# Optimization experiments

Measured on AMD Instinct MI355X. Metric: run time of the kernel, lower is better.

The kernel has to match this reference:

```python
import jax, jax.numpy as jnp
import numpy as np

DIM = 1024
HEADS = 16
HEAD_DIM = DIM // HEADS
SCALE = HEAD_DIM ** -0.5


def setup_inputs() -> dict:
    key = jax.random.key(0)
    ks = jax.random.split(key, 7)
    B, N, M = 2, 2048, 2048
    x = jax.random.normal(ks[0], (B, N, DIM), dtype=jnp.float32)
    y = jax.random.normal(ks[1], (B, M, DIM), dtype=jnp.float32)
    s = DIM ** -0.5
    Wq = jax.random.normal(ks[2], (DIM, DIM), dtype=jnp.float32) * s
    Wk = jax.random.normal(ks[3], (DIM, DIM), dtype=jnp.float32) * s
    Wv = jax.random.normal(ks[4], (DIM, DIM), dtype=jnp.float32) * s
    Wp = jax.random.normal(ks[5], (DIM, DIM), dtype=jnp.float32) * s
    bp = jax.random.normal(ks[6], (DIM,), dtype=jnp.float32) * 0.01
    return {"x": x, "y": y, "Wq": Wq, "Wk": Wk, "Wv": Wv, "Wp": Wp, "bp": bp}


def _split_heads(t):
    b, n, _ = t.shape
    return t.reshape(b, n, HEADS, HEAD_DIM).transpose(0, 2, 1, 3)  # b h n d


def reference(x, y, Wq, Wk, Wv, Wp, bp):
    q = _split_heads(x @ Wq)  # [b,h,n,d]
    k = _split_heads(y @ Wk)  # [b,h,m,d]
    v = _split_heads(y @ Wv)  # [b,h,m,d]
    attn = jnp.einsum('bhid,bhjd->bhij', q, k) * SCALE  # [b,h,n,m]
    attn = jax.nn.softmax(attn, axis=-1)
    out = jnp.einsum('bhij,bhjd->bhid', attn, v)  # [b,h,n,d]
    b, h, n, d = out.shape
    out = out.transpose(0, 2, 1, 3).reshape(b, n, h * d)  # [b,n,dim]
    return out @ Wp + bp
```

## Files before the change

### kernel.cpp

```cpp
#include <hip/hip_runtime.h>
#include <hip/hip_bf16.h>
#include <cstdint>

#define DIM   1024
#define HEADS 16
#define HDIM  64
#define BATCH 2
#define SEQ   2048
#define ROWS  (BATCH*SEQ)
static constexpr float QSCALE = 0.18033688f;

typedef float  f32x4  __attribute__((ext_vector_type(4)));
typedef float  f32x16 __attribute__((ext_vector_type(16)));
typedef float  float4v __attribute__((ext_vector_type(4)));
typedef __bf16 bf16x8 __attribute__((ext_vector_type(8)));
typedef __bf16 bf16x4 __attribute__((ext_vector_type(4)));
typedef __bf16 bf16x2 __attribute__((ext_vector_type(2)));
typedef unsigned u32x4v __attribute__((ext_vector_type(4)));

__device__ __forceinline__ void glds16(const __bf16* g, __bf16* l) {
  __builtin_amdgcn_global_load_lds(
      (const __attribute__((address_space(1))) void*)g,
      (__attribute__((address_space(3))) void*)l, 16, 0, 0);
}

__device__ __forceinline__ void wait_dma0() {
  asm volatile("s_waitcnt vmcnt(0) lgkmcnt(0)" ::: "memory");
}

__global__ __launch_bounds__(256) void prep_kernel(
    const float* __restrict__ x, const float* __restrict__ y,
    const float* __restrict__ Wq, const float* __restrict__ Wk,
    const float* __restrict__ Wv, const float* __restrict__ Wp,
    __bf16* __restrict__ xb, __bf16* __restrict__ yb, __bf16* __restrict__ Wt) {
  const int z = blockIdx.z, t = threadIdx.x;
  const size_t NEL = (size_t)ROWS * DIM;
  if (z < 8) {
    size_t idx = (((size_t)z * 1024 + blockIdx.x) * 256 + t) * 4;
    const float* s; __bf16* d;
    if (idx < NEL) { s = x + idx; d = xb + idx; }
    else           { s = y + (idx - NEL); d = yb + (idx - NEL); }
    const float4v v = *(const float4v*)s;
    bf16x4 o;
    o[0] = (__bf16)v[0]; o[1] = (__bf16)v[1]; o[2] = (__bf16)v[2]; o[3] = (__bf16)v[3];
    *(bf16x4*)d = o;
    return;
  }
  const int w = blockIdx.x >> 8, rem = blockIdx.x & 255;
  const float* W = (w == 0) ? Wq : (w == 1) ? Wk : (w == 2) ? Wv : Wp;
  __bf16* dst = Wt + (size_t)w * DIM * DIM;
  const int n0 = (rem & 15) * 64, k0 = (rem >> 4) * 64;
  __shared__ float T[64][65];
  const int col = t & 63, rw = t >> 6;
  #pragma unroll
  for (int p = 0; p < 16; ++p) {
    const int row = p * 4 + rw;
    T[row][col] = W[(size_t)(k0 + row) * DIM + n0 + col];
  }
  __syncthreads();
  #pragma unroll
  for (int p = 0; p < 16; ++p) {
    const int row = p * 4 + rw;
    dst[(size_t)(n0 + row) * DIM + k0 + col] = (__bf16)T[col][row];
  }
}

__global__ __launch_bounds__(256) void proj_kernel(
    const __bf16* __restrict__ xb, const __bf16* __restrict__ yb,
    const __bf16* __restrict__ Wt,
    __bf16* __restrict__ Qb, __bf16* __restrict__ Kb, __bf16* __restrict__ VT) {
  const int z = blockIdx.z;
  const __bf16* A = (z == 0) ? xb : yb;
  const __bf16* Bt = Wt + (size_t)z * DIM * DIM;

  __shared__ __bf16 S[2][128 * 64];
  __bf16* As = S[0];
  __bf16* Bs = S[1];

  const int t = threadIdx.x, lane = t & 63, wave = t >> 6;
  const int l15 = lane & 15, quad = lane >> 4;
  const int wm = wave & 1, wn = wave >> 1;
  const int rowBase = blockIdx.y * 128, colBase = blockIdx.x * 128;
  const int srow = lane >> 3;
  const int scol = ((lane & 7) ^ srow) * 8;

  f32x4 acc[4][4] = {};

  for (int kb = 0; kb < DIM; kb += 64) {
    __syncthreads();
    #pragma unroll
    for (int i = 0; i < 4; ++i) {
      const int c = wave * 4 + i;
      const int row = c * 8 + srow;
      glds16(&A[(size_t)(rowBase + row) * DIM + kb + scol], &As[c * 512]);
      glds16(&Bt[(size_t)(colBase + row) * DIM + kb + scol], &Bs[c * 512]);
    }
    __syncthreads();
    #pragma unroll
    for (int ks = 0; ks < 2; ++ks) {
      bf16x8 a[4], b[4];
      #pragma unroll
      for (int mi = 0; mi < 4; ++mi) {
        const int row = wm * 64 + mi * 16 + l15;
        a[mi] = *(const bf16x8*)&As[row * 64 + (((ks << 2) | quad) ^ (row & 7)) * 8];
      }
      #pragma unroll
      for (int ni = 0; ni < 4; ++ni) {
        const int row = wn * 64 + ni * 16 + l15;
        b[ni] = *(const bf16x8*)&Bs[row * 64 + (((ks << 2) | quad) ^ (row & 7)) * 8];
      }
      #pragma unroll
      for (int mi = 0; mi < 4; ++mi)
        #pragma unroll
        for (int ni = 0; ni < 4; ++ni)
          acc[mi][ni] = __builtin_amdgcn_mfma_f32_16x16x32_bf16(a[mi], b[ni], acc[mi][ni], 0, 0, 0);
    }
  }

  if (z < 2) {
    __bf16* out = (z == 0) ? Qb : Kb;
    const float sc = (z == 0) ? QSCALE : 1.0f;
    #pragma unroll
    for (int mi = 0; mi < 4; ++mi) {
      const int row0 = rowBase + wm * 64 + mi * 16 + quad * 4;
      #pragma unroll
      for (int ni = 0; ni < 4; ++ni) {
        const int col = colBase + wn * 64 + ni * 16 + l15;
        #pragma unroll
        for (int r = 0; r < 4; ++r)
          out[(size_t)(row0 + r) * DIM + col] = (__bf16)(acc[mi][ni][r] * sc);
      }
    }
    return;
  }

  __syncthreads();
  __bf16* Ts = &S[0][0];
  #pragma unroll
  for (int mi = 0; mi < 4; ++mi) {
    const int bk3 = wm * 8 + mi * 2 + (quad >> 1);
    #pragma unroll
    for (int ni = 0; ni < 4; ++ni) {
      const int dl = wn * 64 + ni * 16 + l15;
      bf16x4 pk;
      #pragma unroll
      for (int r = 0; r < 4; ++r) pk[r] = (__bf16)acc[mi][ni][r];
      *(bf16x4*)&Ts[dl * 128 + (bk3 ^ (dl & 7)) * 8 + (quad & 1) * 4] = pk;
    }
  }
  __syncthreads();
  const int d = t >> 1, khh = t & 1;
  const size_t vrow = (size_t)((rowBase >> 11) * HEADS * HDIM) + colBase + d;
  const int key0g = rowBase & (SEQ - 1);
  #pragma unroll
  for (int j = 0; j < 8; ++j) {
    const int kc = khh * 8 + j;
    const int lc = (kc & 8) | ((kc ^ d) & 7);
    const bf16x8 v = *(const bf16x8*)&Ts[d * 128 + lc * 8];
    *(bf16x8*)&VT[vrow * SEQ + key0g + kc * 8] = v;
  }
}

__global__ __launch_bounds__(256, 2) void attn_kernel(
    const __bf16* __restrict__ Qb, const __bf16* __restrict__ Kb,
    const __bf16* __restrict__ VT, __bf16* __restrict__ Ob) {
  __shared__ __bf16 KV[2][2][64 * 64];

  const int t = threadIdx.x, lane = t & 63, wave = t >> 6;
  const int x = lane & 31, hi = lane >> 5;
  const int bh = blockIdx.y, b = bh >> 4, h = bh & 15;
  const int qbase = blockIdx.x * 128 + wave * 32;
  const int srow = lane >> 3;
  const int scol = ((lane & 7) ^ srow) * 8;

  const __bf16* Kbh = Kb + (size_t)b * SEQ * DIM + h * HDIM;
  const __bf16* Vbh = VT + (size_t)bh * HDIM * SEQ;

  bf16x8 qf[4];
  #pragma unroll
  for (int kd = 0; kd < 4; ++kd)
    qf[kd] = *(const bf16x8*)&Qb[(size_t)(b * SEQ + qbase + x) * DIM
                                 + h * HDIM + kd * 16 + hi * 8];

  f32x16 o0 = {}, o1 = {};
  float lsum = 0.f;

  const int he16 = (hi ^ (x & 7)) << 4;
  const int rowb = x * 128;

  auto stage = [&](int jb, int buf) {
    #pragma unroll
    for (int i = 0; i < 2; ++i) {
      const int c = wave * 2 + i;
      const int row = c * 8 + srow;
      glds16(&Kbh[(size_t)(jb + row) * DIM + scol], &KV[buf][0][c * 512]);
      glds16(&Vbh[(size_t)row * SEQ + jb + scol], &KV[buf][1][c * 512]);
    }
  };

  stage(0, 0);
  for (int j = 0; j < SEQ / 64; ++j) {
    const int buf = j & 1;
    wait_dma0();
    __syncthreads();
    if (j + 1 < SEQ / 64) stage((j + 1) * 64, buf ^ 1);
    const char* Ks = (const char*)KV[buf][0];
    const char* Vs = (const char*)KV[buf][1];

    f32x16 sT0 = {}, sT1 = {};
    #pragma unroll
    for (int kd = 0; kd < 4; ++kd) {
      const bf16x8 kf = *(const bf16x8*)(Ks + rowb + (he16 ^ (kd << 5)));
      sT0 = __builtin_amdgcn_mfma_f32_32x32x16_bf16(kf, qf[kd], sT0, 0, 0, 0);
    }
    #pragma unroll
    for (int kd = 0; kd < 4; ++kd) {
      const bf16x8 kf = *(const bf16x8*)(Ks + 4096 + rowb + (he16 ^ (kd << 5)));
      sT1 = __builtin_amdgcn_mfma_f32_32x32x16_bf16(kf, qf[kd], sT1, 0, 0, 0);
    }

    #pragma unroll
    for (int kt = 0; kt < 2; ++kt) {
      const f32x16 s = kt ? sT1 : sT0;
      unsigned w[8];
      #pragma unroll
      for (int i = 0; i < 8; ++i) {
        const float p0 = __builtin_amdgcn_exp2f(s[2 * i]);
        const float p1 = __builtin_amdgcn_exp2f(s[2 * i + 1]);
        bf16x2 pk; pk[0] = (__bf16)p0; pk[1] = (__bf16)p1;
        const unsigned u = __builtin_bit_cast(unsigned, pk);
        w[i] = u;
        lsum += __builtin_bit_cast(float, u << 16)
              + __builtin_bit_cast(float, u & 0xffff0000u);
      }
#if __has_builtin(__builtin_amdgcn_permlane32_swap)
      const auto s02 = __builtin_amdgcn_permlane32_swap(w[0], w[2], false, false);
      const auto s13 = __builtin_amdgcn_permlane32_swap(w[1], w[3], false, false);
      const auto s46 = __builtin_amdgcn_permlane32_swap(w[4], w[6], false, false);
      const auto s57 = __builtin_amdgcn_permlane32_swap(w[5], w[7], false, false);
      const u32x4v f0v = {(unsigned)s02[0], (unsigned)s13[0], (unsigned)s02[1], (unsigned)s13[1]};
      const u32x4v f1v = {(unsigned)s46[0], (unsigned)s57[0], (unsigned)s46[1], (unsigned)s57[1]};
#else
      const unsigned q0 = __shfl_xor((int)w[0], 32, 64), q1 = __shfl_xor((int)w[1], 32, 64);
      const unsigned q2 = __shfl_xor((int)w[2], 32, 64), q3 = __shfl_xor((int)w[3], 32, 64);
      const unsigned q4 = __shfl_xor((int)w[4], 32, 64), q5 = __shfl_xor((int)w[5], 32, 64);
      const unsigned q6 = __shfl_xor((int)w[6], 32, 64), q7 = __shfl_xor((int)w[7], 32, 64);
      const u32x4v f0v = {hi ? q2 : w[0], hi ? q3 : w[1], hi ? w[2] : q0, hi ? w[3] : q1};
      const u32x4v f1v = {hi ? q6 : w[4], hi ? q7 : w[5], hi ? w[6] : q4, hi ? w[7] : q5};
#endif
      const bf16x8 F0 = __builtin_bit_cast(bf16x8, f0v);
      const bf16x8 F1 = __builtin_bit_cast(bf16x8, f1v);

      const int kb0 = kt << 6;
      {
        const bf16x8 va = *(const bf16x8*)(Vs + rowb + (he16 ^ kb0));
        const bf16x8 vb = *(const bf16x8*)(Vs + 4096 + rowb + (he16 ^ kb0));
        o0 = __builtin_amdgcn_mfma_f32_32x32x16_bf16(F0, va, o0, 0, 0, 0);
        o1 = __builtin_amdgcn_mfma_f32_32x32x16_bf16(F0, vb, o1, 0, 0, 0);
      }
      {
        const bf16x8 va = *(const bf16x8*)(Vs + rowb + (he16 ^ (kb0 | 32)));
        const bf16x8 vb = *(const bf16x8*)(Vs + 4096 + rowb + (he16 ^ (kb0 | 32)));
        o0 = __builtin_amdgcn_mfma_f32_32x32x16_bf16(F1, va, o0, 0, 0, 0);
        o1 = __builtin_amdgcn_mfma_f32_32x32x16_bf16(F1, vb, o1, 0, 0, 0);
      }
    }
  }

  const float ltot = lsum + __shfl_xor(lsum, 32, 64);
  const float linv = 1.f / ltot;
  #pragma unroll
  for (int r = 0; r < 16; ++r) {
    const int q = (r & 3) + 8 * (r >> 2) + 4 * hi;
    const float inv = __shfl(linv, q, 64);
    __bf16* dst = &Ob[(size_t)(b * SEQ + qbase + q) * DIM + h * HDIM + x];
    dst[0]  = (__bf16)(o0[r] * inv);
    dst[32] = (__bf16)(o1[r] * inv);
  }
}

__global__ __launch_bounds__(256) void outproj_kernel(
    const __bf16* __restrict__ A, const __bf16* __restrict__ Bt,
    const float* __restrict__ bias, float* __restrict__ out) {
  __shared__ __bf16 As[64 * 64];
  __shared__ __bf16 Bs[128 * 64];

  const int t = threadIdx.x, lane = t & 63, wave = t >> 6;
  const int l15 = lane & 15, quad = lane >> 4;
  const int wm = wave & 1, wn = wave >> 1;
  const int rowBase = blockIdx.y * 64, colBase = blockIdx.x * 128;
  const int srow = lane >> 3;
  const int scol = ((lane & 7) ^ srow) * 8;

  f32x4 acc[2][4] = {};

  for (int kb = 0; kb < DIM; kb += 64) {
    __syncthreads();
    #pragma unroll
    for (int i = 0; i < 2; ++i) {
      const int c = wave * 2 + i;
      const int row = c * 8 + srow;
      glds16(&A[(size_t)(rowBase + row) * DIM + kb + scol], &As[c * 512]);
    }
    #pragma unroll
    for (int i = 0; i < 4; ++i) {
      const int c = wave * 4 + i;
      const int row = c * 8 + srow;
      glds16(&Bt[(size_t)(colBase + row) * DIM + kb + scol], &Bs[c * 512]);
    }
    __syncthreads();
    #pragma unroll
    for (int ks = 0; ks < 2; ++ks) {
      bf16x8 a[2], b[4];
      #pragma unroll
      for (int mi = 0; mi < 2; ++mi) {
        const int row = wm * 32 + mi * 16 + l15;
        a[mi] = *(const bf16x8*)&As[row * 64 + (((ks << 2) | quad) ^ (row & 7)) * 8];
      }
      #pragma unroll
      for (int ni = 0; ni < 4; ++ni) {
        const int row = wn * 64 + ni * 16 + l15;
        b[ni] = *(const bf16x8*)&Bs[row * 64 + (((ks << 2) | quad) ^ (row & 7)) * 8];
      }
      #pragma unroll
      for (int mi = 0; mi < 2; ++mi)
        #pragma unroll
        for (int ni = 0; ni < 4; ++ni)
          acc[mi][ni] = __builtin_amdgcn_mfma_f32_16x16x32_bf16(a[mi], b[ni], acc[mi][ni], 0, 0, 0);
    }
  }

  #pragma unroll
  for (int mi = 0; mi < 2; ++mi) {
    const int row0 = rowBase + wm * 32 + mi * 16 + quad * 4;
    #pragma unroll
    for (int ni = 0; ni < 4; ++ni) {
      const int col = colBase + wn * 64 + ni * 16 + l15;
      const float bb = bias[col];
      #pragma unroll
      for (int r = 0; r < 4; ++r)
        out[(size_t)(row0 + r) * DIM + col] = acc[mi][ni][r] + bb;
    }
  }
}

extern "C" void kernel_launch(void* const* d_in, const int* in_sizes, int n_in,
                              void* d_out, int out_size, void* d_ws, size_t ws_size,
                              hipStream_t stream) {
  const float* x  = (const float*)d_in[0];
  const float* y  = (const float*)d_in[1];
  const float* Wq = (const float*)d_in[2];
  const float* Wk = (const float*)d_in[3];
  const float* Wv = (const float*)d_in[4];
  const float* Wp = (const float*)d_in[5];
  const float* bp = (const float*)d_in[6];
  float* out = (float*)d_out;

  const size_t NEL = (size_t)ROWS * DIM;
  __bf16* xb = (__bf16*)d_ws;
  __bf16* yb = xb + NEL;
  __bf16* Wt = yb + NEL;
  __bf16* Qb = Wt + NEL;
  __bf16* Kb = Qb + NEL;
  __bf16* VT = Kb + NEL;
  __bf16* Ob = xb;

  prep_kernel<<<dim3(1024, 1, 9), 256, 0, stream>>>(x, y, Wq, Wk, Wv, Wp, xb, yb, Wt);
  proj_kernel<<<dim3(DIM / 128, ROWS / 128, 3), 256, 0, stream>>>(xb, yb, Wt, Qb, Kb, VT);
  attn_kernel<<<dim3(SEQ / 128, BATCH * HEADS), 256, 0, stream>>>(Qb, Kb, VT, Ob);
  outproj_kernel<<<dim3(DIM / 128, ROWS / 64), 256, 0, stream>>>(Ob, Wt + 3 * NEL / 4, bp, out);
}
```

Before: 208.8 us.

## Double-buffer LDS staging in projection GEMMs with block swizzle

```diff
diff --git a/kernel.cpp b/kernel.cpp
--- a/kernel.cpp
+++ b/kernel.cpp
@@ -65,37 +65,46 @@
   }
 }
 
-__global__ __launch_bounds__(256) void proj_kernel(
+__global__ __launch_bounds__(256, 2) void proj_kernel(
     const __bf16* __restrict__ xb, const __bf16* __restrict__ yb,
     const __bf16* __restrict__ Wt,
     __bf16* __restrict__ Qb, __bf16* __restrict__ Kb, __bf16* __restrict__ VT) {
-  const int z = blockIdx.z;
+  const int lin = blockIdx.x + 8 * (blockIdx.y + 32 * blockIdx.z);
+  const int swz = (lin & 7) * 96 + (lin >> 3);
+  const int bx = swz & 7, by = (swz >> 3) & 31, z = swz >> 8;
+
   const __bf16* A = (z == 0) ? xb : yb;
   const __bf16* Bt = Wt + (size_t)z * DIM * DIM;
 
-  __shared__ __bf16 S[2][128 * 64];
-  __bf16* As = S[0];
-  __bf16* Bs = S[1];
+  __shared__ __bf16 S[2][2][128 * 64];
 
   const int t = threadIdx.x, lane = t & 63, wave = t >> 6;
   const int l15 = lane & 15, quad = lane >> 4;
   const int wm = wave & 1, wn = wave >> 1;
-  const int rowBase = blockIdx.y * 128, colBase = blockIdx.x * 128;
+  const int rowBase = by * 128, colBase = bx * 128;
   const int srow = lane >> 3;
   const int scol = ((lane & 7) ^ srow) * 8;
 
   f32x4 acc[4][4] = {};
 
-  for (int kb = 0; kb < DIM; kb += 64) {
-    __syncthreads();
+  auto stage = [&](int kb, int buf) {
     #pragma unroll
     for (int i = 0; i < 4; ++i) {
       const int c = wave * 4 + i;
       const int row = c * 8 + srow;
-      glds16(&A[(size_t)(rowBase + row) * DIM + kb + scol], &As[c * 512]);
-      glds16(&Bt[(size_t)(colBase + row) * DIM + kb + scol], &Bs[c * 512]);
-    }
+      glds16(&A[(size_t)(rowBase + row) * DIM + kb + scol], &S[buf][0][c * 512]);
+      glds16(&Bt[(size_t)(colBase + row) * DIM + kb + scol], &S[buf][1][c * 512]);
+    }
+  };
+
+  stage(0, 0);
+  for (int j = 0; j < DIM / 64; ++j) {
+    const int buf = j & 1;
+    wait_dma0();
     __syncthreads();
+    if (j + 1 < DIM / 64) stage((j + 1) * 64, buf ^ 1);
+    const __bf16* As = S[buf][0];
+    const __bf16* Bs = S[buf][1];
     #pragma unroll
     for (int ks = 0; ks < 2; ++ks) {
       bf16x8 a[4], b[4];
@@ -135,7 +144,7 @@
   }
 
   __syncthreads();
-  __bf16* Ts = &S[0][0];
+  __bf16* Ts = &S[0][0][0];
   #pragma unroll
   for (int mi = 0; mi < 4; ++mi) {
     const int bk3 = wm * 8 + mi * 2 + (quad >> 1);
@@ -279,36 +288,47 @@
   }
 }
 
-__global__ __launch_bounds__(256) void outproj_kernel(
+__global__ __launch_bounds__(256, 2) void outproj_kernel(
     const __bf16* __restrict__ A, const __bf16* __restrict__ Bt,
     const float* __restrict__ bias, float* __restrict__ out) {
-  __shared__ __bf16 As[64 * 64];
-  __shared__ __bf16 Bs[128 * 64];
+  const int lin = blockIdx.x + 8 * blockIdx.y;
+  const int swz = (lin & 7) * 64 + (lin >> 3);
+  const int bx = swz & 7, by = swz >> 3;
+
+  __shared__ __bf16 S[2][12288];
 
   const int t = threadIdx.x, lane = t & 63, wave = t >> 6;
   const int l15 = lane & 15, quad = lane >> 4;
   const int wm = wave & 1, wn = wave >> 1;
-  const int rowBase = blockIdx.y * 64, colBase = blockIdx.x * 128;
+  const int rowBase = by * 64, colBase = bx * 128;
   const int srow = lane >> 3;
   const int scol = ((lane & 7) ^ srow) * 8;
 
   f32x4 acc[2][4] = {};
 
-  for (int kb = 0; kb < DIM; kb += 64) {
-    __syncthreads();
+  auto stage = [&](int kb, int buf) {
     #pragma unroll
     for (int i = 0; i < 2; ++i) {
       const int c = wave * 2 + i;
       const int row = c * 8 + srow;
-      glds16(&A[(size_t)(rowBase + row) * DIM + kb + scol], &As[c * 512]);
+      glds16(&A[(size_t)(rowBase + row) * DIM + kb + scol], &S[buf][c * 512]);
     }
     #pragma unroll
     for (int i = 0; i < 4; ++i) {
       const int c = wave * 4 + i;
       const int row = c * 8 + srow;
-      glds16(&Bt[(size_t)(colBase + row) * DIM + kb + scol], &Bs[c * 512]);
-    }
+      glds16(&Bt[(size_t)(colBase + row) * DIM + kb + scol], &S[buf][4096 + c * 512]);
+    }
+  };
+
+  stage(0, 0);
+  for (int kb = 0; kb < DIM / 64; ++kb) {
+    const int buf = kb & 1;
+    wait_dma0();
     __syncthreads();
+    if (kb + 1 < DIM / 64) stage((kb + 1) * 64, buf ^ 1);
+    const __bf16* As = &S[buf][0];
+    const __bf16* Bs = &S[buf][4096];
     #pragma unroll
     for (int ks = 0; ks < 2; ++ks) {
       bf16x8 a[2], b[4];
```

New measurement: 187.4 us. 1.11x faster.
